# Kernel tuning notes

Measured on AMD Instinct MI355X. Metric: run time of the kernel, lower is better.

Reference implementation:

```python
import jax, jax.numpy as jnp
import numpy as np

TAU = 0.05
A = -0.1
B = 1.1


def setup_inputs() -> dict:
    key = jax.random.key(0)
    ks = jax.random.split(key, 6)
    E = 4_000_000
    N = 100_000
    x = jax.random.normal(ks[0], (N, 128), dtype=jnp.float32)
    edge_index = jax.random.randint(ks[1], (2, E), 0, N, dtype=jnp.int64)
    edge_weight = jax.random.normal(ks[2], (14, E), dtype=jnp.float32)
    # MLP params: Linear(14,7) -> ReLU -> Linear(7,1), torch convention y = x @ W.T + b
    W1 = jax.random.normal(ks[3], (7, 14), dtype=jnp.float32) / np.sqrt(14).astype(np.float32)
    b1 = jnp.zeros((7,), dtype=jnp.float32)
    W2 = jax.random.normal(ks[4], (1, 7), dtype=jnp.float32) / np.sqrt(7).astype(np.float32)
    b2 = jnp.zeros((1,), dtype=jnp.float32)
    # self.random buffer: logit of a uniform sample (Gumbel-ish noise), a scalar
    u = jax.random.uniform(ks[5], (), dtype=jnp.float32, minval=1e-4, maxval=1.0 - 1e-4)
    rand_logit = jnp.log(u) - jnp.log(1.0 - u)
    return {
        "x": x,
        "edge_index": edge_index,
        "edge_weight": edge_weight,
        "W1": W1,
        "b1": b1,
        "W2": W2,
        "b2": b2,
        "rand_logit": rand_logit,
    }


def reference(x, edge_index, edge_weight, W1, b1, W2, b2, rand_logit):
    temp = edge_weight  # [14, E]
    # Faithful to torch: row-major reshape of [14, E] into [E, 14]
    ew = edge_weight.reshape(-1, 14)  # [E, 14]
    h = jax.nn.relu(ew @ W1.T + b1)  # [E, 7]
    s = (h @ W2.T + b2).reshape(-1)  # [E]
    s = jax.nn.sigmoid((rand_logit + s) / TAU)
    v_min = s.min()
    v_max = s.max()
    s = (s - v_min) / (v_max - v_min) * (B - A) + A
    edge_mask = s > 0  # [E] bool
    # Stream compaction (data-dependent shape -> run eagerly, not under jit)
    return edge_index[:, edge_mask], temp[:, edge_mask]
```

## Files before the change

### kernel.cpp

```cpp
#include <hip/hip_runtime.h>
#include <hip/hip_bf16.h>


constexpr int BLOCK = 256;
constexpr int CHUNK = 4096;
constexpr int ROUNDS = CHUNK / BLOCK;

__device__ __forceinline__ bool mask_of(float s, float vmin, float range) {
    float t = __fdiv_rn(__fsub_rn(s, vmin), range);
    float sn = __fadd_rn(__fmul_rn(t, 1.2f), -0.1f);
    return sn > 0.0f;
}


__global__ void k_compute_s(const float* __restrict__ ew,
                            const float* __restrict__ W1, const float* __restrict__ b1,
                            const float* __restrict__ W2, const float* __restrict__ b2,
                            const float* __restrict__ rl,
                            float* __restrict__ s_out,
                            float2* __restrict__ partial,
                            long long E) {
    __shared__ double sW1d[98], sW2d[7];
    __shared__ float sb1[7];
    __shared__ float sb2, srl;
    int tid = threadIdx.x;
    if (tid < 98) sW1d[tid] = (double)W1[tid];
    if (tid < 7) { sW2d[tid] = (double)W2[tid]; sb1[tid] = b1[tid]; }
    if (tid == 0) { sb2 = b2[0]; srl = rl[0]; }
    __syncthreads();

    long long e = (long long)blockIdx.x * BLOCK + tid;
    float lmin = __uint_as_float(0x7F800000u), lmax = 0.0f;

    if (e < E) {
        const float2* p2 = (const float2*)ew + e * 7;
        float2 q0 = p2[0], q1 = p2[1], q2 = p2[2], q3 = p2[3],
               q4 = p2[4], q5 = p2[5], q6 = p2[6];
        float w[14] = {q0.x, q0.y, q1.x, q1.y, q2.x, q2.y, q3.x, q3.y,
                       q4.x, q4.y, q5.x, q5.y, q6.x, q6.y};

        double a0 = 0.0, a1 = 0.0, a2 = 0.0, a3 = 0.0, a4 = 0.0, a5 = 0.0, a6 = 0.0;
#pragma unroll
        for (int j = 0; j < 14; ++j) {
            double fd = (double)w[j];
            a0 += fd * sW1d[0 * 14 + j];
            a1 += fd * sW1d[1 * 14 + j];
            a2 += fd * sW1d[2 * 14 + j];
            a3 += fd * sW1d[3 * 14 + j];
            a4 += fd * sW1d[4 * 14 + j];
            a5 += fd * sW1d[5 * 14 + j];
            a6 += fd * sW1d[6 * 14 + j];
        }
        double acc2 = 0.0;
#define L2STEP(kk, ak) { float hp = __fadd_rn((float)(ak), sb1[kk]); \
                         hp = fmaxf(hp, 0.0f); \
                         acc2 += (double)hp * sW2d[kk]; }
        L2STEP(0, a0) L2STEP(1, a1) L2STEP(2, a2) L2STEP(3, a3)
        L2STEP(4, a4) L2STEP(5, a5) L2STEP(6, a6)
#undef L2STEP
        float raw = __fadd_rn((float)acc2, sb2);
        float z = __fdiv_rn(__fadd_rn(srl, raw), 0.05f);
        float s = __fdiv_rn(1.0f, __fadd_rn(1.0f, expf(-z)));
        s_out[e] = s;
        lmin = s;
        lmax = s;
    }
#pragma unroll
    for (int off = 32; off; off >>= 1) {
        lmin = fminf(lmin, __shfl_down(lmin, off));
        lmax = fmaxf(lmax, __shfl_down(lmax, off));
    }
    __shared__ float wmn[4], wmx[4];
    int lane = tid & 63, wid = tid >> 6;
    if (lane == 0) { wmn[wid] = lmin; wmx[wid] = lmax; }
    __syncthreads();
    if (tid == 0) {
        float m0 = wmn[0], M0 = wmx[0];
#pragma unroll
        for (int q = 1; q < 4; ++q) { m0 = fminf(m0, wmn[q]); M0 = fmaxf(M0, wmx[q]); }
        float2 pr; pr.x = m0; pr.y = M0;
        partial[blockIdx.x] = pr;
    }
}

__global__ void k_minmax(const float2* __restrict__ partial, int n,
                         float* __restrict__ mm) {
    int tid = threadIdx.x;
    float lmin = __uint_as_float(0x7F800000u), lmax = 0.0f;
    for (int i = tid; i < n; i += 1024) {
        float2 p = partial[i];
        lmin = fminf(lmin, p.x);
        lmax = fmaxf(lmax, p.y);
    }
#pragma unroll
    for (int off = 32; off; off >>= 1) {
        lmin = fminf(lmin, __shfl_down(lmin, off));
        lmax = fmaxf(lmax, __shfl_down(lmax, off));
    }
    __shared__ float wmn[16], wmx[16];
    int lane = tid & 63, wid = tid >> 6;
    if (lane == 0) { wmn[wid] = lmin; wmx[wid] = lmax; }
    __syncthreads();
    if (tid == 0) {
        float m = wmn[0], M = wmx[0];
#pragma unroll
        for (int q = 1; q < 16; ++q) { m = fminf(m, wmn[q]); M = fmaxf(M, wmx[q]); }
        mm[0] = m; mm[1] = M;
    }
}

__global__ void k_count(const float* __restrict__ s_arr,
                        const float* __restrict__ mm,
                        int* __restrict__ counts, long long E) {
    int chunk = blockIdx.x;
    long long base = (long long)chunk * CHUNK;
    float vmin = mm[0];
    float range = __fsub_rn(mm[1], vmin);
    int tid = threadIdx.x;
    int cnt = 0;
#pragma unroll
    for (int r = 0; r < ROUNDS; ++r) {
        long long e = base + r * BLOCK + tid;
        if (e < E) cnt += mask_of(s_arr[e], vmin, range) ? 1 : 0;
    }
#pragma unroll
    for (int off = 32; off; off >>= 1) cnt += __shfl_down(cnt, off);
    __shared__ int wc[4];
    if ((tid & 63) == 0) wc[tid >> 6] = cnt;
    __syncthreads();
    if (tid == 0) counts[chunk] = wc[0] + wc[1] + wc[2] + wc[3];
}

__global__ void k_scan(const int* __restrict__ counts, int* __restrict__ offsets,
                       int nchunks) {
    __shared__ int tmp[1024];
    int tid = threadIdx.x;
    int v = (tid < nchunks) ? counts[tid] : 0;
    tmp[tid] = v;
    for (int off = 1; off < 1024; off <<= 1) {
        __syncthreads();
        int y = (tid >= off) ? tmp[tid - off] : 0;
        __syncthreads();
        tmp[tid] += y;
    }
    if (tid < nchunks) offsets[tid] = tmp[tid] - v;
}

__global__ void k_scatter(const float* __restrict__ s_arr,
                          const float* __restrict__ mm,
                          const int* __restrict__ offsets,
                          const int* __restrict__ ei,
                          const float* __restrict__ ew,
                          float* __restrict__ out,
                          long long E, int K) {
    int chunk = blockIdx.x;
    long long base = (long long)chunk * CHUNK;
    int tid = threadIdx.x, lane = tid & 63, wid = tid >> 6;
    float vmin = mm[0];
    float range = __fsub_rn(mm[1], vmin);

    __shared__ int cnt_rw[64];
    __shared__ int off_rw[64];

    for (int r = 0; r < ROUNDS; ++r) {
        long long e = base + r * BLOCK + tid;
        bool m = (e < E) && mask_of(s_arr[e], vmin, range);
        unsigned long long bal = __ballot(m);
        if (lane == 0) cnt_rw[r * 4 + wid] = (int)__popcll(bal);
    }
    __syncthreads();
    if (tid < 64) {
        int v = cnt_rw[tid];
        int x = v;
#pragma unroll
        for (int off = 1; off < 64; off <<= 1) {
            int y = __shfl_up(x, off);
            if (lane >= off) x += y;
        }
        off_rw[tid] = x - v;
    }
    __syncthreads();

    int chunk_base = offsets[chunk];
    unsigned long long lt = (lane == 0) ? 0ull : ((1ull << lane) - 1ull);

    for (int r = 0; r < ROUNDS; ++r) {
        long long e = base + r * BLOCK + tid;
        bool m = (e < E) && mask_of(s_arr[e], vmin, range);
        unsigned long long bal = __ballot(m);
        int myrank = __popcll(bal & lt);
        if (m) {
            long long posl = (long long)chunk_base + off_rw[r * 4 + wid] + myrank;
            if (posl >= 0 && posl < (long long)K) {
                size_t pos = (size_t)posl;
                size_t Ks = (size_t)K;
                out[pos]      = (float)ei[e];
                out[Ks + pos] = (float)ei[E + e];
#pragma unroll
                for (int rr = 0; rr < 14; ++rr)
                    out[(size_t)(2 + rr) * Ks + pos] = ew[(size_t)rr * E + e];
            }
        }
    }
}


extern "C" void kernel_launch(void* const* d_in, const int* in_sizes, int n_in,
                              void* d_out, int out_size, void* d_ws, size_t ws_size,
                              hipStream_t stream) {
    const int*   ei = (const int*)d_in[1];
    const float* ew = (const float*)d_in[2];
    const float* W1 = (const float*)d_in[3];
    const float* b1 = (const float*)d_in[4];
    const float* W2 = (const float*)d_in[5];
    const float* b2 = (const float*)d_in[6];
    const float* rl = (const float*)d_in[7];

    long long E = (long long)in_sizes[2] / 14;
    int K = out_size / 16;
    int nchunks = (int)((E + CHUNK - 1) / CHUNK);
    int nblocks = (int)((E + BLOCK - 1) / BLOCK);

    char* ws = (char*)d_ws;
    float*  s_arr   = (float*)ws;
    float2* partial = (float2*)(ws + (size_t)E * 4);
    float*  mm      = (float*)(ws + (size_t)E * 4 + (size_t)nblocks * 8);
    int*    counts  = (int*)(ws + (size_t)E * 4 + (size_t)nblocks * 8 + 8);
    int*    offsets = counts + nchunks;

    float* out = (float*)d_out;

    k_compute_s<<<nblocks, BLOCK, 0, stream>>>(ew, W1, b1, W2, b2, rl,
                                               s_arr, partial, E);
    k_minmax<<<1, 1024, 0, stream>>>(partial, nblocks, mm);
    k_count<<<nchunks, BLOCK, 0, stream>>>(s_arr, mm, counts, E);
    k_scan<<<1, 1024, 0, stream>>>(counts, offsets, nchunks);
    k_scatter<<<nchunks, BLOCK, 0, stream>>>(s_arr, mm, offsets, ei, ew, out, E, K);
}
```

Baseline: 184.8 us.

## Replace count+scan+scatter with single-pass decoupled look-back scatter

The separate count and scan kernels are merged into the scatter kernel, which now computes each chunk's global offset with decoupled look-back. Blocks take chunk indices from an atomic ticket so they are processed in order, and they publish aggregate and inclusive-prefix flags through a status array. The status array and the ticket are reset inside the compute kernel. This removes two kernel launches and one full read pass over s_arr, at the cost of spin-waiting on predecessor chunks.

```diff
diff --git a/kernel.cpp b/kernel.cpp
--- a/kernel.cpp
+++ b/kernel.cpp
@@ -19,17 +19,24 @@
                             const float* __restrict__ rl,
                             float* __restrict__ s_out,
                             float2* __restrict__ partial,
+                            unsigned long long* __restrict__ status,
+                            unsigned int* __restrict__ ticket,
+                            int nchunks,
                             long long E) {
     __shared__ double sW1d[98], sW2d[7];
     __shared__ float sb1[7];
     __shared__ float sb2, srl;
     int tid = threadIdx.x;
+    long long gidx = (long long)blockIdx.x * BLOCK + tid;
+    if (gidx < nchunks) status[gidx] = 0ULL;
+    if (gidx == nchunks) *ticket = 0u;
+
     if (tid < 98) sW1d[tid] = (double)W1[tid];
     if (tid < 7) { sW2d[tid] = (double)W2[tid]; sb1[tid] = b1[tid]; }
     if (tid == 0) { sb2 = b2[0]; srl = rl[0]; }
     __syncthreads();
 
-    long long e = (long long)blockIdx.x * BLOCK + tid;
+    long long e = gidx;
     float lmin = __uint_as_float(0x7F800000u), lmax = 0.0f;
 
     if (e < E) {
@@ -109,58 +116,27 @@
     }
 }
 
-__global__ void k_count(const float* __restrict__ s_arr,
-                        const float* __restrict__ mm,
-                        int* __restrict__ counts, long long E) {
-    int chunk = blockIdx.x;
+__global__ void k_scatter_lb(const float* __restrict__ s_arr,
+                             const float* __restrict__ mm,
+                             const int* __restrict__ ei,
+                             const float* __restrict__ ew,
+                             float* __restrict__ out,
+                             unsigned long long* __restrict__ status,
+                             unsigned int* __restrict__ ticket,
+                             long long E, int K) {
+    int tid = threadIdx.x, lane = tid & 63, wid = tid >> 6;
+    __shared__ int chunk_s;
+    if (tid == 0) chunk_s = (int)atomicAdd(ticket, 1u);
+    __syncthreads();
+    int chunk = chunk_s;
     long long base = (long long)chunk * CHUNK;
+
     float vmin = mm[0];
     float range = __fsub_rn(mm[1], vmin);
-    int tid = threadIdx.x;
-    int cnt = 0;
-#pragma unroll
-    for (int r = 0; r < ROUNDS; ++r) {
-        long long e = base + r * BLOCK + tid;
-        if (e < E) cnt += mask_of(s_arr[e], vmin, range) ? 1 : 0;
-    }
-#pragma unroll
-    for (int off = 32; off; off >>= 1) cnt += __shfl_down(cnt, off);
-    __shared__ int wc[4];
-    if ((tid & 63) == 0) wc[tid >> 6] = cnt;
-    __syncthreads();
-    if (tid == 0) counts[chunk] = wc[0] + wc[1] + wc[2] + wc[3];
-}
-
-__global__ void k_scan(const int* __restrict__ counts, int* __restrict__ offsets,
-                       int nchunks) {
-    __shared__ int tmp[1024];
-    int tid = threadIdx.x;
-    int v = (tid < nchunks) ? counts[tid] : 0;
-    tmp[tid] = v;
-    for (int off = 1; off < 1024; off <<= 1) {
-        __syncthreads();
-        int y = (tid >= off) ? tmp[tid - off] : 0;
-        __syncthreads();
-        tmp[tid] += y;
-    }
-    if (tid < nchunks) offsets[tid] = tmp[tid] - v;
-}
-
-__global__ void k_scatter(const float* __restrict__ s_arr,
-                          const float* __restrict__ mm,
-                          const int* __restrict__ offsets,
-                          const int* __restrict__ ei,
-                          const float* __restrict__ ew,
-                          float* __restrict__ out,
-                          long long E, int K) {
-    int chunk = blockIdx.x;
-    long long base = (long long)chunk * CHUNK;
-    int tid = threadIdx.x, lane = tid & 63, wid = tid >> 6;
-    float vmin = mm[0];
-    float range = __fsub_rn(mm[1], vmin);
 
     __shared__ int cnt_rw[64];
     __shared__ int off_rw[64];
+    __shared__ int total_s, base_s;
 
     for (int r = 0; r < ROUNDS; ++r) {
         long long e = base + r * BLOCK + tid;
@@ -178,10 +154,51 @@
             if (lane >= off) x += y;
         }
         off_rw[tid] = x - v;
-    }
-    __syncthreads();
-
-    int chunk_base = offsets[chunk];
+        if (tid == 63) total_s = x;
+    }
+    __syncthreads();
+    int total = total_s;
+
+    if (tid == 0 && chunk > 0)
+        atomicExch(&status[chunk], (1ULL << 62) | (unsigned long long)(unsigned)total);
+
+    if (wid == 0) {
+        int prefix = 0;
+        if (chunk > 0) {
+            int j = chunk - 1;
+            while (true) {
+                int idx = j - lane;
+                unsigned flag;
+                unsigned val;
+                if (idx >= 0) {
+                    unsigned long long w = atomicAdd(&status[idx], 0ULL);
+                    flag = (unsigned)(w >> 62);
+                    val  = (unsigned)(w & 0xFFFFFFFFULL);
+                } else { flag = 2u; val = 0u; }
+                unsigned long long b0 = __ballot(flag == 0u);
+                unsigned long long b2 = __ballot(flag == 2u);
+                int p0 = b0 ? (__ffsll((long long)b0) - 1) : 64;
+                int p2 = b2 ? (__ffsll((long long)b2) - 1) : 64;
+                if (p0 < p2) continue;
+                int contrib;
+                if (p2 == 64) contrib = (int)val;
+                else contrib = (lane <= p2) ? (int)val : 0;
+                int sum = contrib;
+#pragma unroll
+                for (int off2 = 32; off2; off2 >>= 1) sum += __shfl_xor(sum, off2);
+                prefix += sum;
+                if (p2 == 64) { j -= 64; continue; }
+                break;
+            }
+        }
+        if (lane == 0) {
+            atomicExch(&status[chunk],
+                       (2ULL << 62) | (unsigned long long)(unsigned)(prefix + total));
+            base_s = prefix;
+        }
+    }
+    __syncthreads();
+    int chunk_base = base_s;
     unsigned long long lt = (lane == 0) ? 0ull : ((1ull << lane) - 1ull);
 
     for (int r = 0; r < ROUNDS; ++r) {
@@ -222,18 +239,18 @@
     int nblocks = (int)((E + BLOCK - 1) / BLOCK);
 
     char* ws = (char*)d_ws;
-    float*  s_arr   = (float*)ws;
-    float2* partial = (float2*)(ws + (size_t)E * 4);
-    float*  mm      = (float*)(ws + (size_t)E * 4 + (size_t)nblocks * 8);
-    int*    counts  = (int*)(ws + (size_t)E * 4 + (size_t)nblocks * 8 + 8);
-    int*    offsets = counts + nchunks;
+    float*              s_arr   = (float*)ws;
+    float2*             partial = (float2*)(ws + (size_t)E * 4);
+    float*              mm      = (float*)(ws + (size_t)E * 4 + (size_t)nblocks * 8);
+    unsigned int*       ticket  = (unsigned int*)(ws + (size_t)E * 4 + (size_t)nblocks * 8 + 8);
+    unsigned long long* status  = (unsigned long long*)(ws + (size_t)E * 4 + (size_t)nblocks * 8 + 16);
 
     float* out = (float*)d_out;
 
     k_compute_s<<<nblocks, BLOCK, 0, stream>>>(ew, W1, b1, W2, b2, rl,
-                                               s_arr, partial, E);
+                                               s_arr, partial, status, ticket,
+                                               nchunks, E);
     k_minmax<<<1, 1024, 0, stream>>>(partial, nblocks, mm);
-    k_count<<<nchunks, BLOCK, 0, stream>>>(s_arr, mm, counts, E);
-    k_scan<<<1, 1024, 0, stream>>>(counts, offsets, nchunks);
-    k_scatter<<<nchunks, BLOCK, 0, stream>>>(s_arr, mm, offsets, ei, ew, out, E, K);
-}
+    k_scatter_lb<<<nchunks, BLOCK, 0, stream>>>(s_arr, mm, ei, ew, out,
+                                                status, ticket, E, K);
+}
```

Result: slower. 258.6 us (+40.0%).

## Store mask ballots in count pass and fold scan into scatter

Applied to the files above, without the earlier changes.

The count kernel now writes each wave's 64-bit mask ballot to workspace, so the scatter kernel reads the ballots instead of re-reading s and recomputing the mask twice. The separate scan kernel is removed: each scatter block sums the counts of all preceding chunks itself with one wave. This drops a kernel launch and two full passes over s (about 16MB of reads). In exchange each block does redundant prefix summing, up to ~1000 counts for later chunks.

```diff
diff --git a/kernel.cpp b/kernel.cpp
--- a/kernel.cpp
+++ b/kernel.cpp
@@ -111,44 +111,33 @@
 
 __global__ void k_count(const float* __restrict__ s_arr,
                         const float* __restrict__ mm,
-                        int* __restrict__ counts, long long E) {
+                        int* __restrict__ counts,
+                        unsigned long long* __restrict__ ballots,
+                        long long E) {
     int chunk = blockIdx.x;
     long long base = (long long)chunk * CHUNK;
     float vmin = mm[0];
     float range = __fsub_rn(mm[1], vmin);
-    int tid = threadIdx.x;
+    int tid = threadIdx.x, lane = tid & 63, wid = tid >> 6;
     int cnt = 0;
 #pragma unroll
     for (int r = 0; r < ROUNDS; ++r) {
         long long e = base + r * BLOCK + tid;
-        if (e < E) cnt += mask_of(s_arr[e], vmin, range) ? 1 : 0;
+        bool m = (e < E) && mask_of(s_arr[e], vmin, range);
+        unsigned long long bal = __ballot(m);
+        if (lane == 0) ballots[(size_t)chunk * 64 + r * 4 + wid] = bal;
+        cnt += m ? 1 : 0;
     }
 #pragma unroll
     for (int off = 32; off; off >>= 1) cnt += __shfl_down(cnt, off);
     __shared__ int wc[4];
-    if ((tid & 63) == 0) wc[tid >> 6] = cnt;
+    if (lane == 0) wc[wid] = cnt;
     __syncthreads();
     if (tid == 0) counts[chunk] = wc[0] + wc[1] + wc[2] + wc[3];
 }
 
-__global__ void k_scan(const int* __restrict__ counts, int* __restrict__ offsets,
-                       int nchunks) {
-    __shared__ int tmp[1024];
-    int tid = threadIdx.x;
-    int v = (tid < nchunks) ? counts[tid] : 0;
-    tmp[tid] = v;
-    for (int off = 1; off < 1024; off <<= 1) {
-        __syncthreads();
-        int y = (tid >= off) ? tmp[tid - off] : 0;
-        __syncthreads();
-        tmp[tid] += y;
-    }
-    if (tid < nchunks) offsets[tid] = tmp[tid] - v;
-}
-
-__global__ void k_scatter(const float* __restrict__ s_arr,
-                          const float* __restrict__ mm,
-                          const int* __restrict__ offsets,
+__global__ void k_scatter(const int* __restrict__ counts,
+                          const unsigned long long* __restrict__ ballots,
                           const int* __restrict__ ei,
                           const float* __restrict__ ew,
                           float* __restrict__ out,
@@ -156,21 +145,23 @@
     int chunk = blockIdx.x;
     long long base = (long long)chunk * CHUNK;
     int tid = threadIdx.x, lane = tid & 63, wid = tid >> 6;
-    float vmin = mm[0];
-    float range = __fsub_rn(mm[1], vmin);
-
-    __shared__ int cnt_rw[64];
+
+    __shared__ unsigned long long sbal[64];
     __shared__ int off_rw[64];
-
-    for (int r = 0; r < ROUNDS; ++r) {
-        long long e = base + r * BLOCK + tid;
-        bool m = (e < E) && mask_of(s_arr[e], vmin, range);
-        unsigned long long bal = __ballot(m);
-        if (lane == 0) cnt_rw[r * 4 + wid] = (int)__popcll(bal);
-    }
-    __syncthreads();
+    __shared__ int base_s;
+
+    unsigned long long mybal = 0ULL;
+    if (tid < 64) { mybal = ballots[(size_t)chunk * 64 + tid]; sbal[tid] = mybal; }
+
+    if (wid == 1) {
+        int sum = 0;
+        for (int i = lane; i < chunk; i += 64) sum += counts[i];
+#pragma unroll
+        for (int off = 32; off; off >>= 1) sum += __shfl_xor(sum, off);
+        if (lane == 0) base_s = sum;
+    }
     if (tid < 64) {
-        int v = cnt_rw[tid];
+        int v = (int)__popcll(mybal);
         int x = v;
 #pragma unroll
         for (int off = 1; off < 64; off <<= 1) {
@@ -181,15 +172,14 @@
     }
     __syncthreads();
 
-    int chunk_base = offsets[chunk];
-    unsigned long long lt = (lane == 0) ? 0ull : ((1ull << lane) - 1ull);
+    int chunk_base = base_s;
 
     for (int r = 0; r < ROUNDS; ++r) {
-        long long e = base + r * BLOCK + tid;
-        bool m = (e < E) && mask_of(s_arr[e], vmin, range);
-        unsigned long long bal = __ballot(m);
-        int myrank = __popcll(bal & lt);
+        unsigned long long bal = sbal[r * 4 + wid];
+        bool m = (bal >> lane) & 1ULL;
         if (m) {
+            long long e = base + r * BLOCK + tid;
+            int myrank = __popcll(bal & ((1ULL << lane) - 1ULL));
             long long posl = (long long)chunk_base + off_rw[r * 4 + wid] + myrank;
             if (posl >= 0 && posl < (long long)K) {
                 size_t pos = (size_t)posl;
@@ -222,18 +212,22 @@
     int nblocks = (int)((E + BLOCK - 1) / BLOCK);
 
     char* ws = (char*)d_ws;
-    float*  s_arr   = (float*)ws;
-    float2* partial = (float2*)(ws + (size_t)E * 4);
-    float*  mm      = (float*)(ws + (size_t)E * 4 + (size_t)nblocks * 8);
-    int*    counts  = (int*)(ws + (size_t)E * 4 + (size_t)nblocks * 8 + 8);
-    int*    offsets = counts + nchunks;
+    size_t off0 = 0;
+    float*  s_arr   = (float*)(ws + off0);
+    size_t off1 = off0 + (size_t)E * 4;
+    float2* partial = (float2*)(ws + off1);
+    size_t off2 = off1 + (size_t)nblocks * 8;
+    float*  mm      = (float*)(ws + off2);
+    size_t off3 = off2 + 8;
+    int*    counts  = (int*)(ws + off3);
+    size_t off4 = (off3 + (size_t)nchunks * 4 + 7) & ~(size_t)7;
+    unsigned long long* ballots = (unsigned long long*)(ws + off4);
 
     float* out = (float*)d_out;
 
     k_compute_s<<<nblocks, BLOCK, 0, stream>>>(ew, W1, b1, W2, b2, rl,
                                                s_arr, partial, E);
     k_minmax<<<1, 1024, 0, stream>>>(partial, nblocks, mm);
-    k_count<<<nchunks, BLOCK, 0, stream>>>(s_arr, mm, counts, E);
-    k_scan<<<1, 1024, 0, stream>>>(counts, offsets, nchunks);
-    k_scatter<<<nchunks, BLOCK, 0, stream>>>(s_arr, mm, offsets, ei, ew, out, E, K);
-}
+    k_count<<<nchunks, BLOCK, 0, stream>>>(s_arr, mm, counts, ballots, E);
+    k_scatter<<<nchunks, BLOCK, 0, stream>>>(counts, ballots, ei, ew, out, E, K);
+}
```

After: 239.6 us. +29.7%, slower.

## Compact chunk indices in LDS and scatter rows with dense coalesced writes

Applied to the files above, without the earlier changes.

The scatter kernel now saves each wavefront's ballot mask in shared memory and builds a compacted list of the surviving edge offsets in LDS, which removes the second pass of s reads and mask evaluation. Output writes then go row by row, with consecutive threads writing consecutive output positions, so stores are fully coalesced instead of spread across the sparse lanes that passed the mask. The gathered reads from the edge-weight rows stay within the chunk's 4096-element window. In exchange it uses about 8KB of extra LDS per block and adds a serial loop over 14 rows.

```diff
diff --git a/kernel.cpp b/kernel.cpp
--- a/kernel.cpp
+++ b/kernel.cpp
@@ -159,18 +159,20 @@
     float vmin = mm[0];
     float range = __fsub_rn(mm[1], vmin);
 
-    __shared__ int cnt_rw[64];
+    __shared__ unsigned long long sbal[64];
     __shared__ int off_rw[64];
+    __shared__ int total_s;
+    __shared__ unsigned short lds_src[CHUNK];
 
     for (int r = 0; r < ROUNDS; ++r) {
         long long e = base + r * BLOCK + tid;
         bool m = (e < E) && mask_of(s_arr[e], vmin, range);
         unsigned long long bal = __ballot(m);
-        if (lane == 0) cnt_rw[r * 4 + wid] = (int)__popcll(bal);
+        if (lane == 0) sbal[r * 4 + wid] = bal;
     }
     __syncthreads();
     if (tid < 64) {
-        int v = cnt_rw[tid];
+        int v = (int)__popcll(sbal[tid]);
         int x = v;
 #pragma unroll
         for (int off = 1; off < 64; off <<= 1) {
@@ -178,28 +180,40 @@
             if (lane >= off) x += y;
         }
         off_rw[tid] = x - v;
-    }
-    __syncthreads();
-
-    int chunk_base = offsets[chunk];
+        if (tid == 63) total_s = x;
+    }
+    __syncthreads();
+
     unsigned long long lt = (lane == 0) ? 0ull : ((1ull << lane) - 1ull);
-
     for (int r = 0; r < ROUNDS; ++r) {
-        long long e = base + r * BLOCK + tid;
-        bool m = (e < E) && mask_of(s_arr[e], vmin, range);
-        unsigned long long bal = __ballot(m);
-        int myrank = __popcll(bal & lt);
-        if (m) {
-            long long posl = (long long)chunk_base + off_rw[r * 4 + wid] + myrank;
-            if (posl >= 0 && posl < (long long)K) {
-                size_t pos = (size_t)posl;
-                size_t Ks = (size_t)K;
-                out[pos]      = (float)ei[e];
-                out[Ks + pos] = (float)ei[E + e];
-#pragma unroll
-                for (int rr = 0; rr < 14; ++rr)
-                    out[(size_t)(2 + rr) * Ks + pos] = ew[(size_t)rr * E + e];
-            }
+        unsigned long long bal = sbal[r * 4 + wid];
+        if ((bal >> lane) & 1ULL) {
+            int rank = __popcll(bal & lt);
+            lds_src[off_rw[r * 4 + wid] + rank] = (unsigned short)(r * BLOCK + tid);
+        }
+    }
+    __syncthreads();
+
+    int total = total_s;
+    long long chunk_base = (long long)offsets[chunk];
+    size_t Ks = (size_t)K;
+
+    for (int idx = tid; idx < total; idx += BLOCK) {
+        long long e = base + lds_src[idx];
+        long long pos = chunk_base + idx;
+        if (pos >= 0 && pos < (long long)K) {
+            out[(size_t)pos]      = (float)ei[e];
+            out[Ks + (size_t)pos] = (float)ei[E + e];
+        }
+    }
+#pragma unroll 1
+    for (int rr = 0; rr < 14; ++rr) {
+        const float* srcrow = ew + (size_t)rr * E + base;
+        float* dstrow = out + (size_t)(2 + rr) * Ks;
+        for (int idx = tid; idx < total; idx += BLOCK) {
+            long long pos = chunk_base + idx;
+            if (pos >= 0 && pos < (long long)K)
+                dstrow[(size_t)pos] = srcrow[lds_src[idx]];
         }
     }
 }
```

Measured after the change: 240.6 us. +30.3%, slower.
